# Optimization experiments

Measured on AMD Instinct MI355X. Metric: run time of the kernel, lower is better.

Reference implementation:

```python
import jax, jax.numpy as jnp
import numpy as np

N_NODES = 100000
N_EDGES = 1000000
M_DIM = 4
HID = 64
N_GRAPHS = 64


def setup_inputs() -> dict:
    key = jax.random.key(0)
    ks = jax.random.split(key, 16)
    x = jax.random.normal(ks[0], (N_NODES, 1, M_DIM), dtype=jnp.float32)
    edge_index = jax.random.randint(ks[1], (2, N_EDGES), 0, N_NODES, dtype=jnp.int64)
    batch = jnp.sort(jax.random.randint(ks[2], (N_NODES,), 0, N_GRAPHS, dtype=jnp.int64))
    def lin(k, out_c, in_c):
        bound = 1.0 / np.sqrt(in_c)
        return jax.random.uniform(k, (out_c, in_c), jnp.float32, -bound, bound)
    inp = {"x": x, "edge_index": edge_index, "batch": batch}
    inp["W1l"] = lin(ks[3], HID, 1); inp["b1l"] = jnp.zeros((HID,), jnp.float32)
    inp["W1r"] = lin(ks[4], HID, 1)
    inp["W2l"] = lin(ks[5], HID, HID); inp["b2l"] = jnp.zeros((HID,), jnp.float32)
    inp["W2r"] = lin(ks[6], HID, HID)
    inp["W3l"] = lin(ks[7], HID, HID); inp["b3l"] = jnp.zeros((HID,), jnp.float32)
    inp["W3r"] = lin(ks[8], HID, HID)
    inp["Wlin"] = lin(ks[9], 1, HID); inp["blin"] = jnp.zeros((1,), jnp.float32)
    return inp


def _sage_conv(x, src, dst, Wl, bl, Wr):
    # x: [N, F, M]; mean aggregation over in-edges, then lin_l/lin_r GEMMs.
    N, F, M = x.shape
    msg = x[src]  # [E, F, M] gather
    s = jax.ops.segment_sum(msg, dst, num_segments=N)
    cnt = jax.ops.segment_sum(jnp.ones((src.shape[0],), x.dtype), dst, num_segments=N)
    agg = s / jnp.maximum(cnt, 1.0)[:, None, None]  # [N, F, M]
    C = Wl.shape[0]
    # torch .view(N*M, F) on contiguous [N,F,M] == row-major reshape (mixes F and M)
    h = (agg.reshape(N * M, F) @ Wl.T + bl).reshape(N, C, M)
    h = h + (x.reshape(N * M, F) @ Wr.T).reshape(N, C, M)
    return h


def reference(x, edge_index, batch, W1l, b1l, W1r, W2l, b2l, W2r, W3l, b3l, W3r, Wlin, blin):
    src, dst = edge_index[0], edge_index[1]
    h = jax.nn.relu(_sage_conv(x, src, dst, W1l, b1l, W1r))
    h = jax.nn.relu(_sage_conv(h, src, dst, W2l, b2l, W2r))
    h = jax.nn.relu(_sage_conv(h, src, dst, W3l, b3l, W3r))
    # new_global_mean_pool: scatter-mean over nodes -> [B, HID, M]
    sums = jax.ops.segment_sum(h, batch, num_segments=N_GRAPHS)
    cnts = jax.ops.segment_sum(jnp.ones((h.shape[0],), h.dtype), batch, num_segments=N_GRAPHS)
    pooled = sums / jnp.maximum(cnts, 1.0)[:, None, None]
    # dropout in eval mode == identity
    B, F, M = pooled.shape
    z = (pooled.reshape(B * M, F) @ Wlin.T + blin).reshape(B, M)
    return jax.nn.sigmoid(z).mean(axis=1)  # [B]
```

## Files before the change

kernel.cpp:

```cpp
#include <hip/hip_runtime.h>
#include <math.h>

#define TPB 256

typedef unsigned short ushort_t;
typedef unsigned char uchar_t;
typedef __attribute__((ext_vector_type(8))) short short8v;
typedef __attribute__((ext_vector_type(4))) float f32x4;
typedef __attribute__((ext_vector_type(8))) unsigned short ushort8;
typedef __attribute__((ext_vector_type(4))) int intv4;

__device__ __forceinline__ unsigned short f2b(float f) {
  union { float f; unsigned int i; } c; c.f = f;
  unsigned int x = c.i;
  x += 0x7FFFu + ((x >> 16) & 1u);
  return (unsigned short)(x >> 16);
}

__device__ __forceinline__ short8v fp8x8_to_bf16(const uchar_t* p) {
  uint2 u = *(const uint2*)p;
  auto p0 = __builtin_amdgcn_cvt_pk_f32_fp8(u.x, false);
  auto p1 = __builtin_amdgcn_cvt_pk_f32_fp8(u.x, true);
  auto p2 = __builtin_amdgcn_cvt_pk_f32_fp8(u.y, false);
  auto p3 = __builtin_amdgcn_cvt_pk_f32_fp8(u.y, true);
  ushort8 o;
  o[0] = f2b(p0[0]); o[1] = f2b(p0[1]); o[2] = f2b(p1[0]); o[3] = f2b(p1[1]);
  o[4] = f2b(p2[0]); o[5] = f2b(p2[1]); o[6] = f2b(p3[0]); o[7] = f2b(p3[1]);
  union { ushort8 a; short8v b; } c; c.a = o; return c.b;
}

__global__ void k_histg(const int* __restrict__ dst, int* deg,
                        const int* __restrict__ batch, int* gcnt, int E, int N) {
  int t = blockIdx.x * TPB + threadIdx.x;
  if (t < E) atomicAdd(&deg[__builtin_nontemporal_load(dst + t)], 1);
  int n0 = t * 16;
  if (n0 < N) {
    int n1 = min(n0 + 16, N);
    int cur = batch[n0];
    int c = 0;
    for (int n = n0; n < n1; ++n) {
      int b = batch[n];
      if (b != cur) { atomicAdd(&gcnt[cur], c); cur = b; c = 0; }
      ++c;
    }
    atomicAdd(&gcnt[cur], c);
  }
}

__global__ void k_scan1(const int* __restrict__ deg, int* rp, int* bsum, int N) {
  __shared__ int s[TPB];
  int t = threadIdx.x;
  int i = blockIdx.x * TPB + t;
  int v = (i < N) ? ((deg[i] + 7) & ~7) : 0;
  s[t] = v;
  __syncthreads();
  for (int d = 1; d < TPB; d <<= 1) {
    int u = (t >= d) ? s[t - d] : 0;
    __syncthreads();
    s[t] += u;
    __syncthreads();
  }
  if (i < N) rp[i] = s[t] - v;
  if (t == TPB - 1) bsum[blockIdx.x] = s[t];
}

__global__ void k_scan2(const int* bsum, int* boff, int nb) {
  __shared__ int s[1024];
  int t = threadIdx.x;
  int v = (t < nb) ? bsum[t] : 0;
  s[t] = v;
  __syncthreads();
  for (int d = 1; d < 1024; d <<= 1) {
    int u = (t >= d) ? s[t - d] : 0;
    __syncthreads();
    s[t] += u;
    __syncthreads();
  }
  if (t < nb) boff[t] = s[t] - v;
}

__global__ void k_scan3(int* rp, const int* __restrict__ boff, const int* __restrict__ bsum,
                        int* cursor, int N, int nb) {
  int i = blockIdx.x * TPB + threadIdx.x;
  if (i < N) {
    int v = rp[i] + boff[i >> 8];
    rp[i] = v;
    cursor[i] = v;
  } else if (i == N) {
    rp[N] = boff[nb - 1] + bsum[nb - 1];
  }
}

__global__ void k_fill(const intv4* __restrict__ src4, const intv4* __restrict__ dst4,
                       int* cursor, int* __restrict__ csr, int E4, int E) {
  int q = blockIdx.x * TPB + threadIdx.x;
  if (q >= E4) return;
  intv4 d = __builtin_nontemporal_load(dst4 + q);
  intv4 s = __builtin_nontemporal_load(src4 + q);
  int base = q * 4;
#pragma unroll
  for (int j = 0; j < 4; ++j) {
    if (base + j < E) {
      int p = atomicAdd(&cursor[d[j]], 1);
      __builtin_nontemporal_store(s[j], csr + p);
    }
  }
}

__global__ void k_cvtw(const float* __restrict__ s0, const float* __restrict__ s1,
                       const float* __restrict__ s2, const float* __restrict__ s3,
                       ushort_t* d0, ushort_t* d1, ushort_t* d2, ushort_t* d3,
                       uchar_t* zr0, int n) {
  int i = blockIdx.x * TPB + threadIdx.x;
  if (i < n) { d0[i] = f2b(s0[i]); d1[i] = f2b(s1[i]); d2[i] = f2b(s2[i]); d3[i] = f2b(s3[i]); }
  if (blockIdx.x == 0 && threadIdx.x < 64) ((int*)zr0)[threadIdx.x] = 0;
}

__global__ void k_agg1(const float4* __restrict__ x, const int* __restrict__ rp,
                       const int* __restrict__ deg, const int* __restrict__ cursor,
                       int* __restrict__ csr, float4* __restrict__ agg1, int N) {
  int n = blockIdx.x * TPB + threadIdx.x;
  if (n >= N) return;
  int b = rp[n], e = rp[n + 1];
  float4 a = make_float4(0.f, 0.f, 0.f, 0.f);
  for (int i = b; i < e; i += 8) {
    int4 c0 = *(const int4*)(csr + i);
    int4 c1 = *(const int4*)(csr + i + 4);
    int id[8] = {c0.x, c0.y, c0.z, c0.w, c1.x, c1.y, c1.z, c1.w};
#pragma unroll
    for (int j = 0; j < 8; ++j) {
      unsigned idx = min((unsigned)id[j], (unsigned)(N - 1));
      float m = ((unsigned)id[j] < (unsigned)N) ? 1.f : 0.f;
      float4 v = x[idx];
      a.x += v.x * m; a.y += v.y * m; a.z += v.z * m; a.w += v.w * m;
    }
  }
  int d = deg[n];
  float inv = (d > 0) ? 1.f / (float)d : 0.f;
  a.x *= inv; a.y *= inv; a.z *= inv; a.w *= inv;
  agg1[n] = a;
  int c = cursor[n];
  for (int p2 = c; p2 < e; ++p2) csr[p2] = N;
}

__global__ __launch_bounds__(256) void k_gemm(
    const uchar_t* __restrict__ hIn8,
    const float* __restrict__ xf, const float* __restrict__ agg1f,
    const float* __restrict__ W1l, const float* __restrict__ b1l,
    const float* __restrict__ W1r,
    const ushort_t* __restrict__ Wlb, const ushort_t* __restrict__ Wrb,
    const float* __restrict__ bias,
    uchar_t* __restrict__ Yl8, uchar_t* __restrict__ Yr8, int rows) {
  int t = threadIdx.x;
  int wave = t >> 6, lane = t & 63;
  int g = lane >> 4, l15 = lane & 15;
  int r0 = blockIdx.x * 64 + wave * 16;
  int r = r0 + l15;

  short8v af0, af1;
  if (hIn8) {
    const uchar_t* hrow = hIn8 + (size_t)r * 64;
    af0 = fp8x8_to_bf16(hrow + g * 8);
    af1 = fp8x8_to_bf16(hrow + 32 + g * 8);
  } else {
    float sA = agg1f[r], sX = xf[r];
    ushort8 o0, o1;
#pragma unroll
    for (int k = 0; k < 8; ++k) {
      int c0 = g * 8 + k, c1 = 32 + g * 8 + k;
      o0[k] = f2b(fmaxf(sA * W1l[c0] + b1l[c0] + sX * W1r[c0], 0.f));
      o1[k] = f2b(fmaxf(sA * W1l[c1] + b1l[c1] + sX * W1r[c1], 0.f));
    }
    union { ushort8 a; short8v b; } u0, u1;
    u0.a = o0; u1.a = o1;
    af0 = u0.b; af1 = u1.b;
  }

#pragma unroll
  for (int c = 0; c < 4; ++c) {
    const ushort_t* wl = Wlb + (size_t)(c * 16 + l15) * 64;
    const ushort_t* wr = Wrb + (size_t)(c * 16 + l15) * 64;
    short8v bl0 = *(const short8v*)(wl + g * 8);
    short8v bl1 = *(const short8v*)(wl + 32 + g * 8);
    short8v br0 = *(const short8v*)(wr + g * 8);
    short8v br1 = *(const short8v*)(wr + 32 + g * 8);
    float bv = bias[c * 16 + l15];
    f32x4 accl = (f32x4){0.f, 0.f, 0.f, 0.f};
    f32x4 accr = (f32x4){bv, bv, bv, bv};
    accl = __builtin_amdgcn_mfma_f32_16x16x32_bf16(af0, bl0, accl, 0, 0, 0);
    accl = __builtin_amdgcn_mfma_f32_16x16x32_bf16(af1, bl1, accl, 0, 0, 0);
    accr = __builtin_amdgcn_mfma_f32_16x16x32_bf16(af0, br0, accr, 0, 0, 0);
    accr = __builtin_amdgcn_mfma_f32_16x16x32_bf16(af1, br1, accr, 0, 0, 0);
#pragma unroll
    for (int i = 0; i < 4; ++i) {
      size_t off = (size_t)(r0 + g * 4 + i) * 64 + c * 16 + l15;
      Yl8[off] = (uchar_t)(__builtin_amdgcn_cvt_pk_fp8_f32(accl[i], accl[i], 0u, false) & 0xFF);
      Yr8[off] = (uchar_t)(__builtin_amdgcn_cvt_pk_fp8_f32(accr[i], accr[i], 0u, false) & 0xFF);
    }
  }
}

#define ADD8(IDX) { \
    uint2 v = *(const uint2*)(base + ((size_t)(unsigned)(IDX) << 8)); \
    auto q0 = __builtin_amdgcn_cvt_pk_f32_fp8(v.x, false); \
    auto q1 = __builtin_amdgcn_cvt_pk_f32_fp8(v.x, true);  \
    auto q2 = __builtin_amdgcn_cvt_pk_f32_fp8(v.y, false); \
    auto q3 = __builtin_amdgcn_cvt_pk_f32_fp8(v.y, true);  \
    acc[0] += q0[0]; acc[1] += q0[1]; acc[2] += q1[0]; acc[3] += q1[1]; \
    acc[4] += q2[0]; acc[5] += q2[1]; acc[6] += q3[0]; acc[7] += q3[1]; }

__global__ __launch_bounds__(256) void k_gather(
    const uchar_t* __restrict__ Yl8, const uchar_t* __restrict__ Yr8,
    const int* __restrict__ rp, const int* __restrict__ deg, const int* __restrict__ csr,
    uchar_t* __restrict__ hOut8, float* __restrict__ pooled,
    const int* __restrict__ batch, int N) {
  __shared__ float ps[1024];
  int tid = blockIdx.x * TPB + threadIdx.x;
  int n = tid >> 5, s = tid & 31;
  bool alive = (n < N);

  float acc[8];
#pragma unroll
  for (int j = 0; j < 8; ++j) acc[j] = 0.f;

  float h[8];
#pragma unroll
  for (int j = 0; j < 8; ++j) h[j] = 0.f;

  if (alive) {
    int b = rp[n], e = rp[n + 1];
    const uchar_t* base = Yl8 + s * 8;
    for (int i = b; i < e; i += 8) {
      int4 c0 = *(const int4*)(csr + i);
      int4 c1 = *(const int4*)(csr + i + 4);
      ADD8(c0.x) ADD8(c0.y) ADD8(c0.z) ADD8(c0.w)
      ADD8(c1.x) ADD8(c1.y) ADD8(c1.z) ADD8(c1.w)
    }
    int d = deg[n];
    float inv = (d > 0) ? 1.f / (float)d : 0.f;
    uint2 yr = *(const uint2*)(Yr8 + (size_t)n * 256 + s * 8);
    auto y0 = __builtin_amdgcn_cvt_pk_f32_fp8(yr.x, false);
    auto y1 = __builtin_amdgcn_cvt_pk_f32_fp8(yr.x, true);
    auto y2 = __builtin_amdgcn_cvt_pk_f32_fp8(yr.y, false);
    auto y3 = __builtin_amdgcn_cvt_pk_f32_fp8(yr.y, true);
    h[0] = fmaxf(acc[0] * inv + y0[0], 0.f);
    h[1] = fmaxf(acc[1] * inv + y0[1], 0.f);
    h[2] = fmaxf(acc[2] * inv + y1[0], 0.f);
    h[3] = fmaxf(acc[3] * inv + y1[1], 0.f);
    h[4] = fmaxf(acc[4] * inv + y2[0], 0.f);
    h[5] = fmaxf(acc[5] * inv + y2[1], 0.f);
    h[6] = fmaxf(acc[6] * inv + y3[0], 0.f);
    h[7] = fmaxf(acc[7] * inv + y3[1], 0.f);
  }

  if (hOut8) {
    if (alive) {
      unsigned int w0 = __builtin_amdgcn_cvt_pk_fp8_f32(h[0], h[1], 0u, false);
      w0 = __builtin_amdgcn_cvt_pk_fp8_f32(h[2], h[3], w0, true);
      unsigned int w1 = __builtin_amdgcn_cvt_pk_fp8_f32(h[4], h[5], 0u, false);
      w1 = __builtin_amdgcn_cvt_pk_fp8_f32(h[6], h[7], w1, true);
      uint2 st; st.x = w0; st.y = w1;
      *(uint2*)(hOut8 + (size_t)n * 256 + s * 8) = st;
    }
    return;
  }

  int nb0 = (blockIdx.x * TPB) >> 5;
  int nlast = min(nb0 + 7, N - 1);
  int bF = batch[nb0], bL = batch[nlast];
  if (bF == bL) {
    int wave = threadIdx.x >> 6;
    int lane = threadIdx.x & 63;
#pragma unroll
    for (int j = 0; j < 8; ++j) h[j] += __shfl_xor(h[j], 32);
    if (lane < 32) {
#pragma unroll
      for (int j = 0; j < 8; ++j) ps[wave * 256 + s * 8 + j] = h[j];
    }
    __syncthreads();
    int t = threadIdx.x;
    if (t < 256) {
      float v = ps[t] + ps[256 + t] + ps[512 + t] + ps[768 + t];
      atomicAdd(&pooled[bF * 256 + t], v);
    }
  } else {
    if (alive) {
      int bb = batch[n];
#pragma unroll
      for (int j = 0; j < 8; ++j)
        atomicAdd(&pooled[bb * 256 + s * 8 + j], h[j]);
    }
  }
}

__global__ void k_final(const float* __restrict__ pooled, const int* __restrict__ gcnt,
                        const float* __restrict__ Wlin, const float* __restrict__ blin,
                        float* __restrict__ out, int B) {
  int t = blockIdx.x * TPB + threadIdx.x;
  int b = t >> 2, j = t & 3;
  if (b >= B) return;
  float inv = 1.f / fmaxf((float)gcnt[b], 1.f);
  float s = blin[0];
  const float* p = pooled + b * 256 + j * 64;
#pragma unroll
  for (int f = 0; f < 64; ++f) s += p[f] * inv * Wlin[f];
  float z = 1.f / (1.f + expf(-s));
  z += __shfl_xor(z, 1);
  z += __shfl_xor(z, 2);
  if (j == 0) out[b] = 0.25f * z;
}

extern "C" void kernel_launch(void* const* d_in, const int* in_sizes, int n_in,
                              void* d_out, int out_size, void* d_ws, size_t ws_size,
                              hipStream_t stream) {
  const float* x   = (const float*)d_in[0];
  const int* edge  = (const int*)d_in[1];
  const int* batch = (const int*)d_in[2];
  const float* W1l = (const float*)d_in[3];
  const float* b1l = (const float*)d_in[4];
  const float* W1r = (const float*)d_in[5];
  const float* W2l = (const float*)d_in[6];
  const float* b2l = (const float*)d_in[7];
  const float* W2r = (const float*)d_in[8];
  const float* W3l = (const float*)d_in[9];
  const float* b3l = (const float*)d_in[10];
  const float* W3r = (const float*)d_in[11];
  const float* Wlin = (const float*)d_in[12];
  const float* blin = (const float*)d_in[13];
  float* out = (float*)d_out;

  const int N = in_sizes[0] / 4;
  const int E = in_sizes[1] / 2;
  const int B = out_size;
  const int rows = 4 * N;

  const int* srcA = edge;
  const int* dstA = edge + E;

  char* p = (char*)d_ws;
  auto carve = [&](size_t bytes) -> void* {
    void* r = (void*)p;
    p += (bytes + 255) & ~(size_t)255;
    return r;
  };
  char* zstart = p;
  int* deg     = (int*)carve((size_t)N * 4);
  int* gcnt    = (int*)carve((size_t)B * 4);
  float* pooled = (float*)carve((size_t)B * 256 * 4);
  size_t zlen  = (size_t)(p - zstart);
  int* rp      = (int*)carve((size_t)(N + 1) * 4);
  int* cursor  = (int*)carve((size_t)N * 4);
  int* bsum    = (int*)carve(4096);
  int* boff    = (int*)carve(4096);
  int* csr     = (int*)carve(((size_t)E + 8 * (size_t)N) * 4);
  float* agg1  = (float*)carve((size_t)N * 4 * 4);
  ushort_t* Wb2l = (ushort_t*)carve(4096 * 2);
  ushort_t* Wb2r = (ushort_t*)carve(4096 * 2);
  ushort_t* Wb3l = (ushort_t*)carve(4096 * 2);
  ushort_t* Wb3r = (ushort_t*)carve(4096 * 2);
  uchar_t* Yl8 = (uchar_t*)carve(((size_t)N + 1) * 256);
  uchar_t* Yr8 = (uchar_t*)carve((size_t)N * 256);
  uchar_t* h8  = (uchar_t*)carve((size_t)N * 256);
  (void)ws_size; (void)n_in;

  hipMemsetAsync(zstart, 0, zlen, stream);

  int nbScan = (N + TPB - 1) / TPB;
  int E4 = (E + 3) / 4;

  k_histg<<<(E + TPB - 1) / TPB, TPB, 0, stream>>>(dstA, deg, batch, gcnt, E, N);
  k_cvtw<<<16, TPB, 0, stream>>>(W2l, W2r, W3l, W3r, Wb2l, Wb2r, Wb3l, Wb3r,
                                 Yl8 + (size_t)N * 256, 4096);
  k_scan1<<<nbScan, TPB, 0, stream>>>(deg, rp, bsum, N);
  k_scan2<<<1, 1024, 0, stream>>>(bsum, boff, nbScan);
  k_scan3<<<(N + 1 + TPB - 1) / TPB, TPB, 0, stream>>>(rp, boff, bsum, cursor, N, nbScan);
  k_fill<<<(E4 + TPB - 1) / TPB, TPB, 0, stream>>>((const intv4*)srcA, (const intv4*)dstA,
                                                   cursor, csr, E4, E);

  k_agg1<<<(N + TPB - 1) / TPB, TPB, 0, stream>>>((const float4*)x, rp, deg, cursor,
                                                  csr, (float4*)agg1, N);

  int nbGemm = (rows + 63) / 64;
  int nbGather = ((size_t)N * 32 + TPB - 1) / TPB;

  k_gemm<<<nbGemm, TPB, 0, stream>>>((const uchar_t*)nullptr, x, agg1, W1l, b1l, W1r,
                                     Wb2l, Wb2r, b2l, Yl8, Yr8, rows);
  k_gather<<<nbGather, TPB, 0, stream>>>(Yl8, Yr8, rp, deg, csr, h8,
                                         (float*)nullptr, batch, N);

  k_gemm<<<nbGemm, TPB, 0, stream>>>(h8, x, agg1, W1l, b1l, W1r,
                                     Wb3l, Wb3r, b3l, Yl8, Yr8, rows);
  k_gather<<<nbGather, TPB, 0, stream>>>(Yl8, Yr8, rp, deg, csr, (uchar_t*)nullptr,
                                         pooled, batch, N);

  k_final<<<(B * 4 + TPB - 1) / TPB, TPB, 0, stream>>>(pooled, gcnt, Wlin, blin, out, B);
}
```

Before: 436.0 us.

## Simplify CSR fill, drop nontemporal hints, tune gather occupancy and early loads

Replaces the vectorized 4-edge-per-thread CSR fill with a one-edge-per-thread kernel using plain loads and stores, and removes the nontemporal load in the degree histogram. In the gather kernel it adds a min-blocks occupancy hint, hoists the degree and root-feature loads ahead of the neighbor loop so their latency overlaps the aggregation, and reuses the accumulator registers for the output instead of a separate array. The goal is more parallelism in the fill and lower register pressure and latency in the gather, at the cost of wider vectorized loads and the cache-bypass hints.

Result: faster. 398.0 us (median of 3 runs) (-8.7%).

```diff
diff --git a/kernel.cpp b/kernel.cpp
--- a/kernel.cpp
+++ b/kernel.cpp
@@ -8,7 +8,6 @@
 typedef __attribute__((ext_vector_type(8))) short short8v;
 typedef __attribute__((ext_vector_type(4))) float f32x4;
 typedef __attribute__((ext_vector_type(8))) unsigned short ushort8;
-typedef __attribute__((ext_vector_type(4))) int intv4;
 
 __device__ __forceinline__ unsigned short f2b(float f) {
   union { float f; unsigned int i; } c; c.f = f;
@@ -32,7 +31,7 @@
 __global__ void k_histg(const int* __restrict__ dst, int* deg,
                         const int* __restrict__ batch, int* gcnt, int E, int N) {
   int t = blockIdx.x * TPB + threadIdx.x;
-  if (t < E) atomicAdd(&deg[__builtin_nontemporal_load(dst + t)], 1);
+  if (t < E) atomicAdd(&deg[dst[t]], 1);
   int n0 = t * 16;
   if (n0 < N) {
     int n1 = min(n0 + 16, N);
@@ -91,19 +90,12 @@
   }
 }
 
-__global__ void k_fill(const intv4* __restrict__ src4, const intv4* __restrict__ dst4,
-                       int* cursor, int* __restrict__ csr, int E4, int E) {
-  int q = blockIdx.x * TPB + threadIdx.x;
-  if (q >= E4) return;
-  intv4 d = __builtin_nontemporal_load(dst4 + q);
-  intv4 s = __builtin_nontemporal_load(src4 + q);
-  int base = q * 4;
-#pragma unroll
-  for (int j = 0; j < 4; ++j) {
-    if (base + j < E) {
-      int p = atomicAdd(&cursor[d[j]], 1);
-      __builtin_nontemporal_store(s[j], csr + p);
-    }
+__global__ void k_fill(const int* __restrict__ src, const int* __restrict__ dst,
+                       int* cursor, int* __restrict__ csr, int E) {
+  int e = blockIdx.x * TPB + threadIdx.x;
+  if (e < E) {
+    int p = atomicAdd(&cursor[dst[e]], 1);
+    csr[p] = src[e];
   }
 }
 
@@ -209,7 +201,7 @@
     acc[0] += q0[0]; acc[1] += q0[1]; acc[2] += q1[0]; acc[3] += q1[1]; \
     acc[4] += q2[0]; acc[5] += q2[1]; acc[6] += q3[0]; acc[7] += q3[1]; }
 
-__global__ __launch_bounds__(256) void k_gather(
+__global__ __launch_bounds__(256, 8) void k_gather(
     const uchar_t* __restrict__ Yl8, const uchar_t* __restrict__ Yr8,
     const int* __restrict__ rp, const int* __restrict__ deg, const int* __restrict__ csr,
     uchar_t* __restrict__ hOut8, float* __restrict__ pooled,
@@ -223,12 +215,10 @@
 #pragma unroll
   for (int j = 0; j < 8; ++j) acc[j] = 0.f;
 
-  float h[8];
-#pragma unroll
-  for (int j = 0; j < 8; ++j) h[j] = 0.f;
-
   if (alive) {
     int b = rp[n], e = rp[n + 1];
+    int d = deg[n];
+    uint2 yr = *(const uint2*)(Yr8 + (size_t)n * 256 + s * 8);
     const uchar_t* base = Yl8 + s * 8;
     for (int i = b; i < e; i += 8) {
       int4 c0 = *(const int4*)(csr + i);
@@ -236,29 +226,27 @@
       ADD8(c0.x) ADD8(c0.y) ADD8(c0.z) ADD8(c0.w)
       ADD8(c1.x) ADD8(c1.y) ADD8(c1.z) ADD8(c1.w)
     }
-    int d = deg[n];
     float inv = (d > 0) ? 1.f / (float)d : 0.f;
-    uint2 yr = *(const uint2*)(Yr8 + (size_t)n * 256 + s * 8);
     auto y0 = __builtin_amdgcn_cvt_pk_f32_fp8(yr.x, false);
     auto y1 = __builtin_amdgcn_cvt_pk_f32_fp8(yr.x, true);
     auto y2 = __builtin_amdgcn_cvt_pk_f32_fp8(yr.y, false);
     auto y3 = __builtin_amdgcn_cvt_pk_f32_fp8(yr.y, true);
-    h[0] = fmaxf(acc[0] * inv + y0[0], 0.f);
-    h[1] = fmaxf(acc[1] * inv + y0[1], 0.f);
-    h[2] = fmaxf(acc[2] * inv + y1[0], 0.f);
-    h[3] = fmaxf(acc[3] * inv + y1[1], 0.f);
-    h[4] = fmaxf(acc[4] * inv + y2[0], 0.f);
-    h[5] = fmaxf(acc[5] * inv + y2[1], 0.f);
-    h[6] = fmaxf(acc[6] * inv + y3[0], 0.f);
-    h[7] = fmaxf(acc[7] * inv + y3[1], 0.f);
+    acc[0] = fmaxf(acc[0] * inv + y0[0], 0.f);
+    acc[1] = fmaxf(acc[1] * inv + y0[1], 0.f);
+    acc[2] = fmaxf(acc[2] * inv + y1[0], 0.f);
+    acc[3] = fmaxf(acc[3] * inv + y1[1], 0.f);
+    acc[4] = fmaxf(acc[4] * inv + y2[0], 0.f);
+    acc[5] = fmaxf(acc[5] * inv + y2[1], 0.f);
+    acc[6] = fmaxf(acc[6] * inv + y3[0], 0.f);
+    acc[7] = fmaxf(acc[7] * inv + y3[1], 0.f);
   }
 
   if (hOut8) {
     if (alive) {
-      unsigned int w0 = __builtin_amdgcn_cvt_pk_fp8_f32(h[0], h[1], 0u, false);
-      w0 = __builtin_amdgcn_cvt_pk_fp8_f32(h[2], h[3], w0, true);
-      unsigned int w1 = __builtin_amdgcn_cvt_pk_fp8_f32(h[4], h[5], 0u, false);
-      w1 = __builtin_amdgcn_cvt_pk_fp8_f32(h[6], h[7], w1, true);
+      unsigned int w0 = __builtin_amdgcn_cvt_pk_fp8_f32(acc[0], acc[1], 0u, false);
+      w0 = __builtin_amdgcn_cvt_pk_fp8_f32(acc[2], acc[3], w0, true);
+      unsigned int w1 = __builtin_amdgcn_cvt_pk_fp8_f32(acc[4], acc[5], 0u, false);
+      w1 = __builtin_amdgcn_cvt_pk_fp8_f32(acc[6], acc[7], w1, true);
       uint2 st; st.x = w0; st.y = w1;
       *(uint2*)(hOut8 + (size_t)n * 256 + s * 8) = st;
     }
@@ -272,23 +260,21 @@
     int wave = threadIdx.x >> 6;
     int lane = threadIdx.x & 63;
 #pragma unroll
-    for (int j = 0; j < 8; ++j) h[j] += __shfl_xor(h[j], 32);
+    for (int j = 0; j < 8; ++j) acc[j] += __shfl_xor(acc[j], 32);
     if (lane < 32) {
 #pragma unroll
-      for (int j = 0; j < 8; ++j) ps[wave * 256 + s * 8 + j] = h[j];
+      for (int j = 0; j < 8; ++j) ps[wave * 256 + s * 8 + j] = acc[j];
     }
     __syncthreads();
     int t = threadIdx.x;
-    if (t < 256) {
-      float v = ps[t] + ps[256 + t] + ps[512 + t] + ps[768 + t];
-      atomicAdd(&pooled[bF * 256 + t], v);
-    }
+    float v = ps[t] + ps[256 + t] + ps[512 + t] + ps[768 + t];
+    atomicAdd(&pooled[bF * 256 + t], v);
   } else {
     if (alive) {
       int bb = batch[n];
 #pragma unroll
       for (int j = 0; j < 8; ++j)
-        atomicAdd(&pooled[bb * 256 + s * 8 + j], h[j]);
+        atomicAdd(&pooled[bb * 256 + s * 8 + j], acc[j]);
     }
   }
 }
@@ -366,7 +352,6 @@
   hipMemsetAsync(zstart, 0, zlen, stream);
 
   int nbScan = (N + TPB - 1) / TPB;
-  int E4 = (E + 3) / 4;
 
   k_histg<<<(E + TPB - 1) / TPB, TPB, 0, stream>>>(dstA, deg, batch, gcnt, E, N);
   k_cvtw<<<16, TPB, 0, stream>>>(W2l, W2r, W3l, W3r, Wb2l, Wb2r, Wb3l, Wb3r,
@@ -374,8 +359,7 @@
   k_scan1<<<nbScan, TPB, 0, stream>>>(deg, rp, bsum, N);
   k_scan2<<<1, 1024, 0, stream>>>(bsum, boff, nbScan);
   k_scan3<<<(N + 1 + TPB - 1) / TPB, TPB, 0, stream>>>(rp, boff, bsum, cursor, N, nbScan);
-  k_fill<<<(E4 + TPB - 1) / TPB, TPB, 0, stream>>>((const intv4*)srcA, (const intv4*)dstA,
-                                                   cursor, csr, E4, E);
+  k_fill<<<(E + TPB - 1) / TPB, TPB, 0, stream>>>(srcA, dstA, cursor, csr, E);
 
   k_agg1<<<(N + TPB - 1) / TPB, TPB, 0, stream>>>((const float4*)x, rp, deg, cursor,
                                                   csr, (float4*)agg1, N);
```
